# Kernel tuning notes

Measured on AMD Instinct MI355X. Metric: run time of the kernel, lower is better.

## Reference

```python
import jax, jax.numpy as jnp
import numpy as np

# tag2index constants
PAD, START, END, T = 0, 14, 15, 16
B, L, V, E, H = 128, 512, 30000, 256, 256


def _lstm(xs, w_ih, w_hh, b, reverse=False):
    """xs: [L, B, E] -> hs: [L, B, H]. PyTorch gate order i,f,g,o."""
    Bsz = xs.shape[1]
    Hd = w_hh.shape[1]
    def cell(carry, xt):
        h, c = carry
        g = xt @ w_ih.T + h @ w_hh.T + b  # [B, 4H]
        i, f, gg, o = jnp.split(g, 4, axis=-1)
        c = jax.nn.sigmoid(f) * c + jax.nn.sigmoid(i) * jnp.tanh(gg)
        h = jax.nn.sigmoid(o) * jnp.tanh(c)
        return (h, c), h
    init = (jnp.zeros((Bsz, Hd), xs.dtype), jnp.zeros((Bsz, Hd), xs.dtype))
    _, hs = jax.lax.scan(cell, init, xs, reverse=reverse)
    return hs


def setup_inputs() -> dict:
    key = jax.random.key(0)
    ks = jax.random.split(key, 12)
    batch_data = jax.random.randint(ks[0], (B, L), 0, V, dtype=jnp.int32)
    # variable-length tags with contiguous trailing PAD (as the model assumes)
    lengths = jax.random.randint(ks[1], (B,), L // 4, L + 1)
    raw_tags = jax.random.randint(ks[2], (B, L), 1, 14, dtype=jnp.int32)  # real tags in [1,14)
    pos = jnp.arange(L)[None, :]
    batch_tag = jnp.where(pos < lengths[:, None], raw_tags, PAD).astype(jnp.int32)
    s = 0.05
    emb = jax.random.normal(ks[3], (V, E), jnp.float32) * s
    w_ih_f = jax.random.normal(ks[4], (4 * H, E), jnp.float32) * s
    w_hh_f = jax.random.normal(ks[5], (4 * H, H), jnp.float32) * s
    b_f = jnp.zeros((4 * H,), jnp.float32)
    w_ih_b = jax.random.normal(ks[6], (4 * H, E), jnp.float32) * s
    w_hh_b = jax.random.normal(ks[7], (4 * H, H), jnp.float32) * s
    b_b = jnp.zeros((4 * H,), jnp.float32)
    w_cls = jax.random.normal(ks[8], (T, 2 * H), jnp.float32) * s
    b_cls = jnp.zeros((T,), jnp.float32)
    transition = jnp.full((T, T), 1.0 / T, jnp.float32)
    return {"batch_data": batch_data, "batch_tag": batch_tag, "emb": emb,
            "w_ih_f": w_ih_f, "w_hh_f": w_hh_f, "b_f": b_f,
            "w_ih_b": w_ih_b, "w_hh_b": w_hh_b, "b_b": b_b,
            "w_cls": w_cls, "b_cls": b_cls, "transition": transition}


def reference(batch_data, batch_tag, emb, w_ih_f, w_hh_f, b_f,
              w_ih_b, w_hh_b, b_b, w_cls, b_cls, transition):
    # ---- BiLSTM encoder ----
    x = emb[batch_data]                      # [B, L, E]
    xs = jnp.moveaxis(x, 1, 0)               # [L, B, E]
    hf = _lstm(xs, w_ih_f, w_hh_f, b_f, reverse=False)
    hb = _lstm(xs, w_ih_b, w_hh_b, b_b, reverse=True)
    out = jnp.moveaxis(jnp.concatenate([hf, hb], axis=-1), 0, 1)  # [B, L, 2H]
    emission = out @ w_cls.T + b_cls          # [B, L, T]
    crf_scores = emission[:, :, None, :] + transition[None, None]  # [B, L, T, T]

    # ---- CRF loss (linear-chain forward algorithm) ----
    mask = batch_tag != PAD                   # [B, L]
    lengths = mask.sum(axis=1)                # [B]
    prev = jnp.concatenate(
        [jnp.full((B, 1), START, batch_tag.dtype), batch_tag[:, :-1]], axis=1)
    idx = (batch_tag + prev * T).astype(jnp.int32)  # flat (prev_tag, cur_tag) index
    flat = crf_scores.reshape(B, L, T * T)
    g = jnp.take_along_axis(flat, idx[:, :, None], axis=2)[..., 0]
    golden_scores = jnp.sum(jnp.where(mask, g, 0.0))

    sc_t = jnp.moveaxis(crf_scores, 1, 0)     # [L, B, T, T]
    init = sc_t[0, :, START, :]               # [B, T] (all lengths >= 1)
    def step(prev_scores, x_t):
        sc, t = x_t
        new = jax.nn.logsumexp(sc + prev_scores[:, :, None], axis=1)  # [B, T]
        active = (lengths > t)[:, None]
        return jnp.where(active, new, prev_scores), None
    final, _ = jax.lax.scan(step, init, (sc_t[1:], jnp.arange(1, L)))
    all_path_scores = jnp.sum(final[:, END])
    loss = (all_path_scores - golden_scores) / B
    return loss
```

## Files before the change

### kernel.cpp

```cpp
#include <hip/hip_runtime.h>

#define Bsz 128
#define Lseq 512
#define Hdim 256
#define Tn 16
#define START_TAG 14
#define END_TAG 15

typedef float f32x4 __attribute__((ext_vector_type(4)));
typedef short s16x8 __attribute__((ext_vector_type(8)));

__device__ __forceinline__ unsigned short f2bf(float f) {
    unsigned int u = __builtin_bit_cast(unsigned int, f);
    u += 0x7fffu + ((u >> 16) & 1u);
    return (unsigned short)(u >> 16);
}
__device__ __forceinline__ float bf2f(unsigned int bits16) {
    return __builtin_bit_cast(float, bits16 << 16);
}
__device__ __forceinline__ float sigmoidf_(float x) {
    return 1.0f / (1.0f + __expf(-x));
}

__global__ void embprep_kernel(const float* __restrict__ emb,
                               unsigned int* __restrict__ embb, int n2) {
    int i = blockIdx.x * blockDim.x + threadIdx.x;
    int stride = gridDim.x * blockDim.x;
    for (; i < n2; i += stride)
        embb[i] = (unsigned int)f2bf(emb[2 * i]) | ((unsigned int)f2bf(emb[2 * i + 1]) << 16);
}

__global__ void wprep_kernel(const float* __restrict__ wih_f, const float* __restrict__ whh_f,
                             const float* __restrict__ wih_b, const float* __restrict__ whh_b,
                             unsigned int* __restrict__ wtile) {
    int bid = blockIdx.x;
    int ki  = bid & 15;
    int tl  = (bid >> 4) & 3;
    int ug  = (bid >> 6) & 15;
    int dir = bid >> 10;
    int t = threadIdx.x;
    int lane = t >> 2, j = t & 3;
    int n = lane & 15, kq = lane >> 4;
    int k0 = ki * 32 + kq * 8 + 2 * j;
    int col = tl * 256 + ug * 16 + n;
    const float* wih = dir ? wih_b : wih_f;
    const float* whh = dir ? whh_b : whh_f;
    float f0, f1;
    if (k0 < 256) { f0 = wih[col * 256 + k0];       f1 = wih[col * 256 + k0 + 1]; }
    else          { f0 = whh[col * 256 + k0 - 256]; f1 = whh[col * 256 + k0 - 255]; }
    wtile[(size_t)bid * 256 + t] = (unsigned int)f2bf(f0) | ((unsigned int)f2bf(f1) << 16);
}

__global__ void lengths_kernel(const int* __restrict__ tag, int* __restrict__ lengths) {
    int b = blockIdx.x;
    int tid = threadIdx.x;
    int cnt = 0;
    for (int l = tid; l < Lseq; l += blockDim.x)
        cnt += (tag[b * Lseq + l] != 0) ? 1 : 0;
    for (int off = 32; off > 0; off >>= 1) cnt += __shfl_down(cnt, off);
    __shared__ int red[4];
    if ((tid & 63) == 0) red[tid >> 6] = cnt;
    __syncthreads();
    if (tid == 0) lengths[b] = red[0] + red[1] + red[2] + red[3];
}

__global__ __launch_bounds__(256, 1) void bilstm_persist(
    const int* __restrict__ bd,
    const unsigned int* __restrict__ embb,
    const unsigned int* __restrict__ wtile,
    const float* __restrict__ b_f, const float* __restrict__ b_b,
    const float* __restrict__ w_cls,
    float* __restrict__ em_f, float* __restrict__ em_b,
    unsigned long long* __restrict__ ring)
{
    const int wg  = blockIdx.x;
    const int dir = wg >> 7;
    const int bg  = (wg >> 4) & 7;
    const int ug  = wg & 15;
    const int tid = threadIdx.x;
    const int gb0 = bg * 16;

    __shared__ unsigned int w_lds[16384];
    __shared__ unsigned int h_lds[16 * 132];
    __shared__ float g_lds[4][16][17];
    __shared__ float part_lds[16][17];
    __shared__ float bias_lds[64];
    __shared__ float wcls_lds[256];

    {
        const unsigned int* wsrc = wtile + ((size_t)(dir * 16 + ug) << 14);
        for (int i = 0; i < 16; ++i) {
            int idx = tid + 256 * i;
            uint4 v4 = *(const uint4*)(wsrc + (size_t)idx * 4);
            *(uint4*)&w_lds[idx * 4] = v4;
        }
        if (tid < 64) {
            const float* bias = dir ? b_b : b_f;
            bias_lds[tid] = bias[(tid >> 4) * 256 + ug * 16 + (tid & 15)];
        }
        wcls_lds[tid] = w_cls[(size_t)ug * (2 * Hdim) + dir * Hdim + tid];
        for (int i = tid; i < 16 * 132; i += 256) h_lds[i] = 0;
    }

    const int wv = tid >> 6;
    const int l  = tid & 63;
    const int n  = l & 15;
    const int kq = l >> 4;
    const int cb = tid >> 4, cu = tid & 15;
    const int em_m = tid >> 4, em_seg = tid & 15;
    const int hm = tid >> 4, hj0 = (tid & 15) * 8;
    float c_reg = 0.f;
    float* emout = dir ? em_b : em_f;
    const int* bd_row = bd + (size_t)(gb0 + n) * Lseq;

    unsigned long long* rbase = ring + (size_t)dir * 2 * 16384;

    __syncthreads();

    f32x4 acc_x = {0.f, 0.f, 0.f, 0.f};
    {
        const int t0 = dir ? (Lseq - 1) : 0;
        int tok = bd_row[t0];
        const unsigned int* xsrc = embb + (size_t)tok * 128 + kq * 4;
        #pragma unroll
        for (int ki = 0; ki < 8; ++ki) {
            uint4 xv = *(const uint4*)(xsrc + ki * 16);
            s16x8 a = __builtin_bit_cast(s16x8, xv);
            s16x8 b = *(const s16x8*)&w_lds[((wv * 16 + ki) * 64 + l) * 4];
            acc_x = __builtin_amdgcn_mfma_f32_16x16x32_bf16(a, b, acc_x, 0, 0, 0);
        }
    }
    int tok_next = (Lseq > 1) ? bd_row[dir ? (Lseq - 2) : 1] : 0;

    unsigned long long v[8];

    for (int s = 0; s < Lseq; ++s) {
        if (s > 0) {
            #pragma unroll
            for (int j = 0; j < 8; ++j)
                h_lds[hm * 132 + hj0 + j] = (unsigned int)v[j];
        }
        __syncthreads();

        if (s > 0) {
            const unsigned int* hr = &h_lds[em_m * 132 + em_seg * 8];
            const float* wc = &wcls_lds[em_seg * 16];
            float p = 0.f;
            #pragma unroll
            for (int j = 0; j < 8; ++j) {
                unsigned int w = hr[j];
                p += bf2f(w & 0xffffu) * wc[2 * j] + bf2f(w >> 16) * wc[2 * j + 1];
            }
            part_lds[em_m][em_seg] = p;
        }
        {
            f32x4 acc = acc_x;
            #pragma unroll
            for (int kih = 0; kih < 8; ++kih) {
                s16x8 a = *(const s16x8*)&h_lds[n * 132 + kih * 16 + kq * 4];
                s16x8 b = *(const s16x8*)&w_lds[(((wv * 16) + 8 + kih) * 64 + l) * 4];
                acc = __builtin_amdgcn_mfma_f32_16x16x32_bf16(a, b, acc, 0, 0, 0);
            }
            #pragma unroll
            for (int r = 0; r < 4; ++r)
                g_lds[wv][kq * 4 + r][n] = acc[r];
        }
        __syncthreads();

        {
            float gi = g_lds[0][cb][cu] + bias_lds[cu];
            float gf = g_lds[1][cb][cu] + bias_lds[16 + cu];
            float gg = g_lds[2][cb][cu] + bias_lds[32 + cu];
            float go = g_lds[3][cb][cu] + bias_lds[48 + cu];
            float cn = sigmoidf_(gf) * c_reg + sigmoidf_(gi) * tanhf(gg);
            c_reg = cn;
            float hn = sigmoidf_(go) * tanhf(cn);
            unsigned int hbits = (unsigned int)f2bf(hn);
            unsigned int other = (unsigned int)__shfl_down((int)hbits, 1);
            if ((cu & 1) == 0) {
                unsigned long long pk = (unsigned long long)(hbits | (other << 16))
                                      | ((unsigned long long)(s + 1) << 32);
                __hip_atomic_store(
                    rbase + ((size_t)(s & 1) * 16384) + (size_t)(gb0 + cb) * 128 + ug * 8 + (cu >> 1),
                    pk, __ATOMIC_RELAXED, __HIP_MEMORY_SCOPE_AGENT);
            }
        }
        if (s > 0 && tid < 16) {
            float ssum = 0.f;
            #pragma unroll
            for (int q = 0; q < 16; ++q) ssum += part_lds[tid][q];
            int t_prev = dir ? (Lseq - s) : (s - 1);
            emout[((size_t)(gb0 + tid) * Lseq + t_prev) * Tn + ug] = ssum;
        }

        if (s + 1 < Lseq) {
            const unsigned int* xsrc = embb + (size_t)tok_next * 128 + kq * 4;
            f32x4 ax = {0.f, 0.f, 0.f, 0.f};
            #pragma unroll
            for (int ki = 0; ki < 8; ++ki) {
                uint4 xv = *(const uint4*)(xsrc + ki * 16);
                s16x8 a = __builtin_bit_cast(s16x8, xv);
                s16x8 b = *(const s16x8*)&w_lds[((wv * 16 + ki) * 64 + l) * 4];
                ax = __builtin_amdgcn_mfma_f32_16x16x32_bf16(a, b, ax, 0, 0, 0);
            }
            acc_x = ax;
        }
        if (s + 2 < Lseq)
            tok_next = bd_row[dir ? (Lseq - 3 - s) : (s + 2)];

        const unsigned long long* src =
            rbase + ((size_t)(s & 1) * 16384) + (size_t)(gb0 + hm) * 128 + hj0;
        #pragma unroll
        for (int j = 0; j < 8; ++j)
            v[j] = __hip_atomic_load(src + j, __ATOMIC_RELAXED, __HIP_MEMORY_SCOPE_AGENT);

        {
            const unsigned long long want = (unsigned long long)(s + 1);
            unsigned int pend = 0xffu;
            while (true) {
                #pragma unroll
                for (int j = 0; j < 8; ++j)
                    if ((pend & (1u << j)) && ((v[j] >> 32) == want))
                        pend &= ~(1u << j);
                if (!pend) break;
                __builtin_amdgcn_s_sleep(2);
                #pragma unroll
                for (int j = 0; j < 8; ++j)
                    if (pend & (1u << j))
                        v[j] = __hip_atomic_load(src + j, __ATOMIC_RELAXED,
                                                 __HIP_MEMORY_SCOPE_AGENT);
            }
        }
    }

    {
        #pragma unroll
        for (int j = 0; j < 8; ++j)
            h_lds[hm * 132 + hj0 + j] = (unsigned int)v[j];
        __syncthreads();
        {
            const unsigned int* hr = &h_lds[em_m * 132 + em_seg * 8];
            const float* wc = &wcls_lds[em_seg * 16];
            float p = 0.f;
            #pragma unroll
            for (int j = 0; j < 8; ++j) {
                unsigned int vv = hr[j];
                p += bf2f(vv & 0xffffu) * wc[2 * j] + bf2f(vv >> 16) * wc[2 * j + 1];
            }
            part_lds[em_m][em_seg] = p;
        }
        __syncthreads();
        if (tid < 16) {
            float ssum = 0.f;
            #pragma unroll
            for (int q = 0; q < 16; ++q) ssum += part_lds[tid][q];
            int t_tail = dir ? 0 : (Lseq - 1);
            emout[((size_t)(gb0 + tid) * Lseq + t_tail) * Tn + ug] = ssum;
        }
    }
}

__global__ void golden_kernel(const int* __restrict__ tag,
                              const float* __restrict__ em_f,
                              const float* __restrict__ em_b,
                              const float* __restrict__ b_cls,
                              const float* __restrict__ trans,
                              float* __restrict__ golden)
{
    int b = blockIdx.x;
    int tid = threadIdx.x;
    float s = 0.f;
    for (int l = tid; l < Lseq; l += blockDim.x) {
        int tg = tag[b * Lseq + l];
        if (tg != 0) {
            int prev = (l == 0) ? START_TAG : tag[b * Lseq + l - 1];
            size_t e = ((size_t)b * Lseq + l) * Tn + tg;
            s += em_f[e] + em_b[e] + b_cls[tg] + trans[prev * Tn + tg];
        }
    }
    for (int off = 32; off > 0; off >>= 1) s += __shfl_down(s, off);
    __shared__ float red[4];
    if ((tid & 63) == 0) red[tid >> 6] = s;
    __syncthreads();
    if (tid == 0) atomicAdd(golden, red[0] + red[1] + red[2] + red[3]);
}

__global__ void crf_forward_kernel(const float* __restrict__ em_f,
                                   const float* __restrict__ em_b,
                                   const float* __restrict__ b_cls,
                                   const float* __restrict__ trans,
                                   const int* __restrict__ lengths,
                                   float* __restrict__ allpath)
{
    int b = blockIdx.x;
    int lane = threadIdx.x;
    int j = lane & 15;
    float tcol[16];
    #pragma unroll
    for (int i = 0; i < 16; ++i) tcol[i] = trans[i * Tn + j];
    float bc = b_cls[j];
    size_t e0 = ((size_t)b * Lseq) * Tn + j;
    float alpha = em_f[e0] + em_b[e0] + bc + tcol[START_TAG];
    int len = lengths[b];
    for (int t = 1; t < Lseq; ++t) {
        float av[16];
        float m = -1e30f;
        #pragma unroll
        for (int i = 0; i < 16; ++i) {
            av[i] = __shfl(alpha, i) + tcol[i];
            m = fmaxf(m, av[i]);
        }
        float sum = 0.f;
        #pragma unroll
        for (int i = 0; i < 16; ++i) sum += __expf(av[i] - m);
        size_t e = ((size_t)b * Lseq + t) * Tn + j;
        float nv = em_f[e] + em_b[e] + bc + m + __logf(sum);
        alpha = (t < len) ? nv : alpha;
    }
    if (lane == END_TAG) atomicAdd(allpath, alpha);
}

__global__ void finalize_kernel(const float* __restrict__ scal, float* __restrict__ out) {
    out[0] = (scal[1] - scal[0]) / (float)Bsz;
}

extern "C" void kernel_launch(void* const* d_in, const int* in_sizes, int n_in,
                              void* d_out, int out_size, void* d_ws, size_t ws_size,
                              hipStream_t stream)
{
    (void)in_sizes; (void)n_in; (void)out_size; (void)ws_size;
    const int*   bd     = (const int*)d_in[0];
    const int*   tag    = (const int*)d_in[1];
    const float* emb    = (const float*)d_in[2];
    const float* w_ih_f = (const float*)d_in[3];
    const float* w_hh_f = (const float*)d_in[4];
    const float* b_f    = (const float*)d_in[5];
    const float* w_ih_b = (const float*)d_in[6];
    const float* w_hh_b = (const float*)d_in[7];
    const float* b_b    = (const float*)d_in[8];
    const float* w_cls  = (const float*)d_in[9];
    const float* b_cls  = (const float*)d_in[10];
    const float* trans  = (const float*)d_in[11];
    float* out = (float*)d_out;

    float* ws = (float*)d_ws;
    float* em_f = ws;
    float* em_b = em_f + (size_t)Bsz * Lseq * Tn;
    unsigned long long* ring =
        (unsigned long long*)(em_b + (size_t)Bsz * Lseq * Tn);
    float* scal = (float*)(ring + 65536);
    int* lengths = (int*)(scal + 8);
    unsigned int* wtile = (unsigned int*)(lengths + 128);
    unsigned int* embb = wtile + (size_t)524288;

    hipMemsetAsync(ring, 0, 65536 * 8 + 8 * sizeof(float), stream);

    embprep_kernel<<<2048, 256, 0, stream>>>(emb, embb, 30000 * 128);
    wprep_kernel<<<2048, 256, 0, stream>>>(w_ih_f, w_hh_f, w_ih_b, w_hh_b, wtile);
    lengths_kernel<<<Bsz, 256, 0, stream>>>(tag, lengths);

    void* kargs[] = {
        (void*)&bd, (void*)&embb, (void*)&wtile,
        (void*)&b_f, (void*)&b_b, (void*)&w_cls,
        (void*)&em_f, (void*)&em_b,
        (void*)&ring
    };
    hipLaunchCooperativeKernel((const void*)bilstm_persist,
                               dim3(256), dim3(256), kargs, 0, stream);

    golden_kernel<<<Bsz, 256, 0, stream>>>(tag, em_f, em_b, b_cls, trans, scal);
    crf_forward_kernel<<<Bsz, 64, 0, stream>>>(em_f, em_b, b_cls, trans, lengths, scal + 1);
    finalize_kernel<<<1, 1, 0, stream>>>(scal, out);
}
```

Before: 2.234 ms.

## Halve persistent LSTM grid by giving each workgroup two hidden-unit groups

Each workgroup of the cooperative BiLSTM kernel now owns two 16-unit hidden slices instead of one, so the grid shrinks from 256 to 128 workgroups and LDS weights double to 128KB. Fewer workgroups take part in the per-step cross-workgroup ring handshake, which is meant to cut synchronization latency on the serial recurrence. In exchange each workgroup does twice the MFMA, gate and classifier work per step, lengthening the critical path inside a step.

```diff
diff --git a/kernel.cpp b/kernel.cpp
--- a/kernel.cpp
+++ b/kernel.cpp
@@ -74,33 +74,36 @@
     unsigned long long* __restrict__ ring)
 {
     const int wg  = blockIdx.x;
-    const int dir = wg >> 7;
-    const int bg  = (wg >> 4) & 7;
-    const int ug  = wg & 15;
+    const int dir = wg >> 6;
+    const int bg  = (wg >> 3) & 7;
+    const int ug2 = wg & 7;
     const int tid = threadIdx.x;
     const int gb0 = bg * 16;
 
-    __shared__ unsigned int w_lds[16384];
+    __shared__ unsigned int w_lds[32768];
     __shared__ unsigned int h_lds[16 * 132];
-    __shared__ float g_lds[4][16][17];
-    __shared__ float part_lds[16][17];
-    __shared__ float bias_lds[64];
-    __shared__ float wcls_lds[256];
-
-    {
-        const unsigned int* wsrc = wtile + ((size_t)(dir * 16 + ug) << 14);
+    __shared__ float g_lds[4][16][33];
+    __shared__ float part_lds[2][16][17];
+    __shared__ float bias_lds[128];
+    __shared__ float wcls_lds[512];
+
+    #pragma unroll
+    for (int u01 = 0; u01 < 2; ++u01) {
+        const unsigned int* wsrc = wtile + ((size_t)(dir * 16 + ug2 * 2 + u01) << 14);
         for (int i = 0; i < 16; ++i) {
             int idx = tid + 256 * i;
             uint4 v4 = *(const uint4*)(wsrc + (size_t)idx * 4);
-            *(uint4*)&w_lds[idx * 4] = v4;
-        }
-        if (tid < 64) {
-            const float* bias = dir ? b_b : b_f;
-            bias_lds[tid] = bias[(tid >> 4) * 256 + ug * 16 + (tid & 15)];
-        }
-        wcls_lds[tid] = w_cls[(size_t)ug * (2 * Hdim) + dir * Hdim + tid];
-        for (int i = tid; i < 16 * 132; i += 256) h_lds[i] = 0;
-    }
+            *(uint4*)&w_lds[(u01 * 4096 + idx) * 4] = v4;
+        }
+    }
+    if (tid < 128) {
+        const float* bias = dir ? b_b : b_f;
+        int u01 = tid >> 6, g = (tid >> 4) & 3, u = tid & 15;
+        bias_lds[tid] = bias[g * 256 + (ug2 * 2 + u01) * 16 + u];
+    }
+    for (int i = tid; i < 512; i += 256)
+        wcls_lds[i] = w_cls[(size_t)(ug2 * 2 + (i >> 8)) * (2 * Hdim) + dir * Hdim + (i & 255)];
+    for (int i = tid; i < 16 * 132; i += 256) h_lds[i] = 0;
 
     const int wv = tid >> 6;
     const int l  = tid & 63;
@@ -109,7 +112,7 @@
     const int cb = tid >> 4, cu = tid & 15;
     const int em_m = tid >> 4, em_seg = tid & 15;
     const int hm = tid >> 4, hj0 = (tid & 15) * 8;
-    float c_reg = 0.f;
+    float c_reg[2] = {0.f, 0.f};
     float* emout = dir ? em_b : em_f;
     const int* bd_row = bd + (size_t)(gb0 + n) * Lseq;
 
@@ -117,17 +120,22 @@
 
     __syncthreads();
 
-    f32x4 acc_x = {0.f, 0.f, 0.f, 0.f};
+    f32x4 acc_x[2];
     {
         const int t0 = dir ? (Lseq - 1) : 0;
         int tok = bd_row[t0];
         const unsigned int* xsrc = embb + (size_t)tok * 128 + kq * 4;
+        acc_x[0] = (f32x4){0.f, 0.f, 0.f, 0.f};
+        acc_x[1] = (f32x4){0.f, 0.f, 0.f, 0.f};
         #pragma unroll
         for (int ki = 0; ki < 8; ++ki) {
             uint4 xv = *(const uint4*)(xsrc + ki * 16);
             s16x8 a = __builtin_bit_cast(s16x8, xv);
-            s16x8 b = *(const s16x8*)&w_lds[((wv * 16 + ki) * 64 + l) * 4];
-            acc_x = __builtin_amdgcn_mfma_f32_16x16x32_bf16(a, b, acc_x, 0, 0, 0);
+            #pragma unroll
+            for (int u01 = 0; u01 < 2; ++u01) {
+                s16x8 b = *(const s16x8*)&w_lds[u01 * 16384 + ((wv * 16 + ki) * 64 + l) * 4];
+                acc_x[u01] = __builtin_amdgcn_mfma_f32_16x16x32_bf16(a, b, acc_x[u01], 0, 0, 0);
+            }
         }
     }
     int tok_next = (Lseq > 1) ? bd_row[dir ? (Lseq - 2) : 1] : 0;
@@ -144,66 +152,84 @@
 
         if (s > 0) {
             const unsigned int* hr = &h_lds[em_m * 132 + em_seg * 8];
-            const float* wc = &wcls_lds[em_seg * 16];
-            float p = 0.f;
-            #pragma unroll
-            for (int j = 0; j < 8; ++j) {
-                unsigned int w = hr[j];
-                p += bf2f(w & 0xffffu) * wc[2 * j] + bf2f(w >> 16) * wc[2 * j + 1];
-            }
-            part_lds[em_m][em_seg] = p;
+            #pragma unroll
+            for (int tg01 = 0; tg01 < 2; ++tg01) {
+                const float* wc = &wcls_lds[tg01 * 256 + em_seg * 16];
+                float p = 0.f;
+                #pragma unroll
+                for (int j = 0; j < 8; ++j) {
+                    unsigned int w = hr[j];
+                    p += bf2f(w & 0xffffu) * wc[2 * j] + bf2f(w >> 16) * wc[2 * j + 1];
+                }
+                part_lds[tg01][em_m][em_seg] = p;
+            }
         }
         {
-            f32x4 acc = acc_x;
+            f32x4 acc0 = acc_x[0], acc1 = acc_x[1];
             #pragma unroll
             for (int kih = 0; kih < 8; ++kih) {
                 s16x8 a = *(const s16x8*)&h_lds[n * 132 + kih * 16 + kq * 4];
-                s16x8 b = *(const s16x8*)&w_lds[(((wv * 16) + 8 + kih) * 64 + l) * 4];
-                acc = __builtin_amdgcn_mfma_f32_16x16x32_bf16(a, b, acc, 0, 0, 0);
-            }
-            #pragma unroll
-            for (int r = 0; r < 4; ++r)
-                g_lds[wv][kq * 4 + r][n] = acc[r];
+                s16x8 b0 = *(const s16x8*)&w_lds[((wv * 16 + 8 + kih) * 64 + l) * 4];
+                s16x8 b1 = *(const s16x8*)&w_lds[16384 + ((wv * 16 + 8 + kih) * 64 + l) * 4];
+                acc0 = __builtin_amdgcn_mfma_f32_16x16x32_bf16(a, b0, acc0, 0, 0, 0);
+                acc1 = __builtin_amdgcn_mfma_f32_16x16x32_bf16(a, b1, acc1, 0, 0, 0);
+            }
+            #pragma unroll
+            for (int r = 0; r < 4; ++r) {
+                g_lds[wv][kq * 4 + r][n]      = acc0[r];
+                g_lds[wv][kq * 4 + r][16 + n] = acc1[r];
+            }
         }
         __syncthreads();
 
         {
-            float gi = g_lds[0][cb][cu] + bias_lds[cu];
-            float gf = g_lds[1][cb][cu] + bias_lds[16 + cu];
-            float gg = g_lds[2][cb][cu] + bias_lds[32 + cu];
-            float go = g_lds[3][cb][cu] + bias_lds[48 + cu];
-            float cn = sigmoidf_(gf) * c_reg + sigmoidf_(gi) * tanhf(gg);
-            c_reg = cn;
-            float hn = sigmoidf_(go) * tanhf(cn);
-            unsigned int hbits = (unsigned int)f2bf(hn);
-            unsigned int other = (unsigned int)__shfl_down((int)hbits, 1);
-            if ((cu & 1) == 0) {
-                unsigned long long pk = (unsigned long long)(hbits | (other << 16))
-                                      | ((unsigned long long)(s + 1) << 32);
-                __hip_atomic_store(
-                    rbase + ((size_t)(s & 1) * 16384) + (size_t)(gb0 + cb) * 128 + ug * 8 + (cu >> 1),
-                    pk, __ATOMIC_RELAXED, __HIP_MEMORY_SCOPE_AGENT);
-            }
-        }
-        if (s > 0 && tid < 16) {
+            const unsigned int tagv = (unsigned int)(s + 1);
+            #pragma unroll
+            for (int u01 = 0; u01 < 2; ++u01) {
+                int uc = u01 * 16 + cu;
+                float gi = g_lds[0][cb][uc] + bias_lds[u01 * 64 + cu];
+                float gf = g_lds[1][cb][uc] + bias_lds[u01 * 64 + 16 + cu];
+                float gg = g_lds[2][cb][uc] + bias_lds[u01 * 64 + 32 + cu];
+                float go = g_lds[3][cb][uc] + bias_lds[u01 * 64 + 48 + cu];
+                float cn = sigmoidf_(gf) * c_reg[u01] + sigmoidf_(gi) * tanhf(gg);
+                c_reg[u01] = cn;
+                float hn = sigmoidf_(go) * tanhf(cn);
+                unsigned int hbits = (unsigned int)f2bf(hn);
+                unsigned int other = (unsigned int)__shfl_down((int)hbits, 1);
+                if ((cu & 1) == 0) {
+                    unsigned long long pk = (unsigned long long)(hbits | (other << 16))
+                                          | ((unsigned long long)tagv << 32);
+                    __hip_atomic_store(
+                        rbase + ((size_t)(s & 1) * 16384) + (size_t)(gb0 + cb) * 128
+                              + ug2 * 16 + u01 * 8 + (cu >> 1),
+                        pk, __ATOMIC_RELAXED, __HIP_MEMORY_SCOPE_AGENT);
+                }
+            }
+        }
+        if (s > 0 && tid < 32) {
+            int m = tid & 15, tg01 = tid >> 4;
             float ssum = 0.f;
             #pragma unroll
-            for (int q = 0; q < 16; ++q) ssum += part_lds[tid][q];
+            for (int q = 0; q < 16; ++q) ssum += part_lds[tg01][m][q];
             int t_prev = dir ? (Lseq - s) : (s - 1);
-            emout[((size_t)(gb0 + tid) * Lseq + t_prev) * Tn + ug] = ssum;
+            emout[((size_t)(gb0 + m) * Lseq + t_prev) * Tn + (ug2 * 2 + tg01)] = ssum;
         }
 
         if (s + 1 < Lseq) {
             const unsigned int* xsrc = embb + (size_t)tok_next * 128 + kq * 4;
-            f32x4 ax = {0.f, 0.f, 0.f, 0.f};
+            f32x4 ax0 = {0.f, 0.f, 0.f, 0.f};
+            f32x4 ax1 = {0.f, 0.f, 0.f, 0.f};
             #pragma unroll
             for (int ki = 0; ki < 8; ++ki) {
                 uint4 xv = *(const uint4*)(xsrc + ki * 16);
                 s16x8 a = __builtin_bit_cast(s16x8, xv);
-                s16x8 b = *(const s16x8*)&w_lds[((wv * 16 + ki) * 64 + l) * 4];
-                ax = __builtin_amdgcn_mfma_f32_16x16x32_bf16(a, b, ax, 0, 0, 0);
-            }
-            acc_x = ax;
+                s16x8 b0 = *(const s16x8*)&w_lds[((wv * 16 + ki) * 64 + l) * 4];
+                s16x8 b1 = *(const s16x8*)&w_lds[16384 + ((wv * 16 + ki) * 64 + l) * 4];
+                ax0 = __builtin_amdgcn_mfma_f32_16x16x32_bf16(a, b0, ax0, 0, 0, 0);
+                ax1 = __builtin_amdgcn_mfma_f32_16x16x32_bf16(a, b1, ax1, 0, 0, 0);
+            }
+            acc_x[0] = ax0;
+            acc_x[1] = ax1;
         }
         if (s + 2 < Lseq)
             tok_next = bd_row[dir ? (Lseq - 3 - s) : (s + 2)];
@@ -240,22 +266,26 @@
         __syncthreads();
         {
             const unsigned int* hr = &h_lds[em_m * 132 + em_seg * 8];
-            const float* wc = &wcls_lds[em_seg * 16];
-            float p = 0.f;
-            #pragma unroll
-            for (int j = 0; j < 8; ++j) {
-                unsigned int vv = hr[j];
-                p += bf2f(vv & 0xffffu) * wc[2 * j] + bf2f(vv >> 16) * wc[2 * j + 1];
-            }
-            part_lds[em_m][em_seg] = p;
+            #pragma unroll
+            for (int tg01 = 0; tg01 < 2; ++tg01) {
+                const float* wc = &wcls_lds[tg01 * 256 + em_seg * 16];
+                float p = 0.f;
+                #pragma unroll
+                for (int j = 0; j < 8; ++j) {
+                    unsigned int vv = hr[j];
+                    p += bf2f(vv & 0xffffu) * wc[2 * j] + bf2f(vv >> 16) * wc[2 * j + 1];
+                }
+                part_lds[tg01][em_m][em_seg] = p;
+            }
         }
         __syncthreads();
-        if (tid < 16) {
+        if (tid < 32) {
+            int m = tid & 15, tg01 = tid >> 4;
             float ssum = 0.f;
             #pragma unroll
-            for (int q = 0; q < 16; ++q) ssum += part_lds[tid][q];
+            for (int q = 0; q < 16; ++q) ssum += part_lds[tg01][m][q];
             int t_tail = dir ? 0 : (Lseq - 1);
-            emout[((size_t)(gb0 + tid) * Lseq + t_tail) * Tn + ug] = ssum;
+            emout[((size_t)(gb0 + m) * Lseq + t_tail) * Tn + (ug2 * 2 + tg01)] = ssum;
         }
     }
 }
@@ -366,7 +396,7 @@
         (void*)&ring
     };
     hipLaunchCooperativeKernel((const void*)bilstm_persist,
-                               dim3(256), dim3(256), kargs, 0, stream);
+                               dim3(128), dim3(256), kargs, 0, stream);
 
     golden_kernel<<<Bsz, 256, 0, stream>>>(tag, em_f, em_b, b_cls, trans, scal);
     crf_forward_kernel<<<Bsz, 64, 0, stream>>>(em_f, em_b, b_cls, trans, lengths, scal + 1);
```

After: 2.540 ms. 1.14x slower.
